# Performance work log

Measured on AMD Instinct MI355X. Metric: run time of the kernel, lower is better.

## Reference

```python
import jax, jax.numpy as jnp
import numpy as np

N = 50000
E = 800000
P = 400000
D_IN = 128
D_HID = 128


def setup_inputs() -> dict:
    key = jax.random.key(0)
    k = jax.random.split(key, 7)
    edge_index = jax.random.randint(k[0], (2, E), 0, N, dtype=jnp.int32)
    edge_pairs = jax.random.randint(k[1], (2, P), 0, N, dtype=jnp.int32)
    emb = jax.random.normal(k[2], (N, D_IN), dtype=jnp.float32)
    W1 = jax.random.normal(k[3], (D_IN, D_HID), dtype=jnp.float32) * (1.0 / np.sqrt(D_IN))
    b1 = jnp.zeros((D_HID,), dtype=jnp.float32)
    W2 = jax.random.normal(k[4], (D_HID, D_HID), dtype=jnp.float32) * (1.0 / np.sqrt(D_HID))
    b2 = jnp.zeros((D_HID,), dtype=jnp.float32)
    return {"edge_index": edge_index, "edge_pairs": edge_pairs, "emb": emb,
            "W1": W1, "b1": b1, "W2": W2, "b2": b2}


def gcn_conv(x, W, b, src, dst):
    """PyG GCNConv: add self-loops, symmetric deg^-1/2 normalization,
    linear transform, scatter-add aggregation into destination nodes."""
    n = x.shape[0]
    loop = jnp.arange(n, dtype=src.dtype)
    s = jnp.concatenate([src, loop])  # [E+N]
    d = jnp.concatenate([dst, loop])
    deg = jax.ops.segment_sum(jnp.ones_like(d, dtype=x.dtype), d, num_segments=n)
    dinv = jnp.where(deg > 0, jax.lax.rsqrt(jnp.maximum(deg, 1e-12)), 0.0)
    norm = dinv[s] * dinv[d]  # [E+N]
    h = x @ W  # [N, out]
    msg = h[s] * norm[:, None]  # gather + scale
    out = jax.ops.segment_sum(msg, d, num_segments=n)  # scatter-add
    return out + b


def reference(edge_index, edge_pairs, emb, W1, b1, W2, b2):
    src, dst = edge_index[0], edge_index[1]
    # encode (eval mode: dropout is identity)
    z = jax.nn.relu(gcn_conv(emb, W1, b1, src, dst))
    z = gcn_conv(z, W2, b2, src, dst)
    # decode: dot product per candidate pair
    return jnp.sum(z[edge_pairs[0]] * z[edge_pairs[1]], axis=1)  # [P]
```

## Files before the change

kernel.cpp:

```cpp
#include <hip/hip_runtime.h>


typedef __attribute__((ext_vector_type(8))) short short8;
typedef __attribute__((ext_vector_type(4))) float floatx4;

#define STAGE_G 128

__device__ __forceinline__ unsigned short f2bf(float f) {
    union { float f; unsigned int u; } v; v.f = f;
    unsigned int u = v.u;
    u += 0x7fffu + ((u >> 16) & 1u);
    return (unsigned short)(u >> 16);
}

__device__ __forceinline__ unsigned int pack2(float a, float b) {
    return (unsigned int)f2bf(a) | ((unsigned int)f2bf(b) << 16);
}

__device__ __forceinline__ float4 cvt4(unsigned int lo, unsigned int hi) {
    float4 f;
    f.x = __uint_as_float(lo << 16);
    f.y = __uint_as_float(lo & 0xffff0000u);
    f.z = __uint_as_float(hi << 16);
    f.w = __uint_as_float(hi & 0xffff0000u);
    return f;
}


__global__ __launch_bounds__(256) void block_hist_kernel(const int* __restrict__ dst,
                                                         int* __restrict__ bhist,
                                                         int E, int NB) {
    __shared__ int bh[1024];
    int t = threadIdx.x, g = blockIdx.x;
    for (int b = t; b < NB; b += 256) bh[b] = 0;
    __syncthreads();
    int chunk = (E + gridDim.x - 1) / gridDim.x;
    int lo = g * chunk, hi = min(lo + chunk, E);
    for (int i = lo + t; i < hi; i += 256) atomicAdd(&bh[dst[i] >> 6], 1);
    __syncthreads();
    for (int b = t; b < NB; b += 256) bhist[g * NB + b] = bh[b];
}

__global__ __launch_bounds__(128) void s1_scan_blocks(int* __restrict__ bhist,
                                                      int* __restrict__ T, int NB) {
    __shared__ int s[2][128];
    int b = blockIdx.x, t = threadIdx.x;
    int v = bhist[t * NB + b];
    int cur = 0;
    s[0][t] = v;
    __syncthreads();
#pragma unroll
    for (int off = 1; off < 128; off <<= 1) {
        int nxt = cur ^ 1;
        int val = s[cur][t];
        if (t >= off) val += s[cur][t - off];
        s[nxt][t] = val;
        __syncthreads();
        cur = nxt;
    }
    int inc = s[cur][t];
    bhist[t * NB + b] = inc - v;
    if (t == 127) T[b] = inc;
}

__global__ __launch_bounds__(256) void stage_kernel(const int* __restrict__ src,
                                                    const int* __restrict__ dst,
                                                    const int* __restrict__ bhist,
                                                    const int* __restrict__ T,
                                                    int* __restrict__ bucket_base,
                                                    unsigned int* __restrict__ stage,
                                                    int E, int NB) {
    __shared__ int lcur[1024];
    __shared__ int sb[2][256];
    int t = threadIdx.x, g = blockIdx.x;

    int b0 = t * 4;
    int v[4];
    int s = 0;
#pragma unroll
    for (int i = 0; i < 4; ++i) {
        int b = b0 + i;
        v[i] = (b < NB) ? T[b] : 0;
        s += v[i];
    }
    int cur = 0;
    sb[0][t] = s;
    __syncthreads();
#pragma unroll
    for (int off = 1; off < 256; off <<= 1) {
        int val = sb[cur][t];
        if (t >= off) val += sb[cur][t - off];
        sb[cur ^ 1][t] = val;
        __syncthreads();
        cur ^= 1;
    }
    int run = sb[cur][t] - s;
#pragma unroll
    for (int i = 0; i < 4; ++i) {
        int b = b0 + i;
        if (b < NB) {
            lcur[b] = run + bhist[(size_t)g * NB + b];
            if (g == 0) bucket_base[b] = run;
        }
        run += v[i];
    }
    if (g == 0 && t == 255) bucket_base[NB] = run;
    __syncthreads();

    int chunk = (E + gridDim.x - 1) / gridDim.x;
    int lo = g * chunk, hi = min(lo + chunk, E);
    for (int i = lo + t; i < hi; i += 256) {
        int d = dst[i];
        int pos = atomicAdd(&lcur[d >> 6], 1);
        stage[pos] = ((unsigned int)src[i] << 6) | (unsigned int)(d & 63);
    }
}

__global__ __launch_bounds__(256) void scatter_kernel(const unsigned int* __restrict__ stage,
                                                      const int* __restrict__ bucket_base,
                                                      int* __restrict__ row_ptr,
                                                      float* __restrict__ dinv,
                                                      int* __restrict__ srcs_sorted,
                                                      int N) {
    __shared__ int cnt[64];
    __shared__ int lcur[64];
    int b = blockIdx.x, t = threadIdx.x;
    int lo = b << 6;
    int base = bucket_base[b], basen = bucket_base[b + 1];
    if (t < 64) cnt[t] = 0;
    __syncthreads();
    for (int i = base + t; i < basen; i += 256) atomicAdd(&cnt[stage[i] & 63u], 1);
    __syncthreads();
    if (t < 64) {
        int v = cnt[t];
        int inc = v;
#pragma unroll
        for (int off = 1; off < 64; off <<= 1) {
            int x = __shfl_up(inc, off, 64);
            if (t >= off) inc += x;
        }
        int exc = inc - v;
        int node = lo + t;
        if (node < N) {
            row_ptr[node] = base + exc;
            dinv[node] = rsqrtf((float)(v + 1));
            if (node == N - 1) row_ptr[N] = base + exc + v;
        }
        lcur[t] = base + exc;
    }
    __syncthreads();
    for (int i = base + t; i < basen; i += 256) {
        unsigned int rec = stage[i];
        int pos = atomicAdd(&lcur[rec & 63u], 1);
        srcs_sorted[pos] = (int)(rec >> 6);
    }
}

__global__ __launch_bounds__(256) void gemm_mfma_kernel(const float* __restrict__ Xv,
                                                        const float* __restrict__ W,
                                                        const float* __restrict__ dinv,
                                                        uint2* __restrict__ H, int N) {
    __shared__ __align__(16) char smem[50176];
    short* WB = (short*)smem;
    short* XL = (short*)(smem + 32768);
    float* Cst = (float*)smem;

    const int tid = threadIdx.x;
    const int w = tid >> 6;
    const int lane = tid & 63;
    const int blk = blockIdx.x;

    {
        const float4* W4 = (const float4*)W;
#pragma unroll
        for (int i = 0; i < 16; ++i) {
            int f = tid + i * 256;
            int k = f >> 5;
            int c4 = f & 31;
            float4 wv = W4[f];
            int kt = k >> 5, q = (k >> 3) & 3, j = k & 7;
            float e[4] = {wv.x, wv.y, wv.z, wv.w};
#pragma unroll
            for (int m = 0; m < 4; ++m) {
                int c = c4 * 4 + m;
                int nt = c >> 4;
                int ln = q * 16 + (c & 15);
                WB[((nt * 4 + kt) * 64 + ln) * 8 + j] = (short)f2bf(e[m]);
            }
        }
    }
    {
#pragma unroll
        for (int i = 0; i < 8; ++i) {
            int f = tid + i * 256;
            int row = f >> 5;
            int c4 = f & 31;
            int gr = min(blk * 64 + row, N - 1);
            float4 xv = ((const float4*)Xv)[(size_t)gr * 32 + c4];
            uint2 u;
            u.x = pack2(xv.x, xv.y);
            u.y = pack2(xv.z, xv.w);
            *(uint2*)&XL[row * 136 + c4 * 4] = u;
        }
    }
    __syncthreads();

    const int arow = w * 16 + (lane & 15);
    const int koff = (lane >> 4) * 8;
    short8 a[4];
#pragma unroll
    for (int kt = 0; kt < 4; ++kt)
        a[kt] = *(const short8*)&XL[arow * 136 + kt * 32 + koff];

    floatx4 acc[8];
#pragma unroll
    for (int nt = 0; nt < 8; ++nt) acc[nt] = (floatx4){0.f, 0.f, 0.f, 0.f};

#pragma unroll
    for (int kt = 0; kt < 4; ++kt) {
#pragma unroll
        for (int nt = 0; nt < 8; ++nt) {
            short8 b = *(const short8*)&WB[((nt * 4 + kt) * 64 + lane) * 8];
            acc[nt] = __builtin_amdgcn_mfma_f32_16x16x32_bf16(a[kt], b, acc[nt], 0, 0, 0);
        }
    }
    __syncthreads();

    {
        int q = lane >> 4, cn = lane & 15;
#pragma unroll
        for (int nt = 0; nt < 8; ++nt)
#pragma unroll
            for (int r = 0; r < 4; ++r)
                Cst[(w * 16 + q * 4 + r) * 132 + nt * 16 + cn] = acc[nt][r];
    }
    __syncthreads();
    {
#pragma unroll
        for (int i = 0; i < 8; ++i) {
            int f = tid + i * 256;
            int row = f >> 5;
            int c4 = f & 31;
            int gr = blk * 64 + row;
            if (gr < N) {
                float4 v = *(float4*)&Cst[row * 132 + c4 * 4];
                float di = dinv[gr];
                uint2 o;
                o.x = pack2(v.x * di, v.y * di);
                o.y = pack2(v.z * di, v.w * di);
                H[(size_t)gr * 32 + c4] = o;
            }
        }
    }
}

__global__ __launch_bounds__(256) void agg_gemm_kernel(const unsigned short* __restrict__ Hp,
                                                       const int* __restrict__ row_ptr,
                                                       const int* __restrict__ srcs,
                                                       const float* __restrict__ dinv,
                                                       const float* __restrict__ bias1,
                                                       const float* __restrict__ W2,
                                                       uint2* __restrict__ Hout, int N) {
    __shared__ __align__(16) char smem[50176];
    short* WB = (short*)smem;
    short* XL = (short*)(smem + 32768);
    float* Cst = (float*)smem;

    const int tid = threadIdx.x;
    const int blk = blockIdx.x;

    {
        const float4* W4 = (const float4*)W2;
#pragma unroll
        for (int i = 0; i < 16; ++i) {
            int f = tid + i * 256;
            int k = f >> 5;
            int c4 = f & 31;
            float4 wv = W4[f];
            int kt = k >> 5, q = (k >> 3) & 3, j = k & 7;
            float e[4] = {wv.x, wv.y, wv.z, wv.w};
#pragma unroll
            for (int m = 0; m < 4; ++m) {
                int c = c4 * 4 + m;
                int nt = c >> 4;
                int ln = q * 16 + (c & 15);
                WB[((nt * 4 + kt) * 64 + ln) * 8 + j] = (short)f2bf(e[m]);
            }
        }
    }

    {
        int qw = tid >> 4;
        int hl = tid & 15;
        const uint4* H4 = (const uint4*)Hp;
        float4 bv0 = ((const float4*)bias1)[2 * hl];
        float4 bv1 = ((const float4*)bias1)[2 * hl + 1];
#pragma unroll
        for (int r = 0; r < 4; ++r) {
            int idx = qw + 16 * r;
            int n = blk * 64 + idx;
            uint4 o;
            if (n < N) {
                uint4 us = H4[(size_t)n * 16 + hl];
                float4 a0 = cvt4(us.x, us.y);
                float4 a1 = cvt4(us.z, us.w);
                float4 c0 = make_float4(0.f, 0.f, 0.f, 0.f);
                float4 c1 = make_float4(0.f, 0.f, 0.f, 0.f);
                int j = row_ptr[n], end = row_ptr[n + 1];
                for (; j + 3 < end; j += 4) {
                    uint4 u0 = H4[(size_t)srcs[j + 0] * 16 + hl];
                    uint4 u1 = H4[(size_t)srcs[j + 1] * 16 + hl];
                    uint4 u2 = H4[(size_t)srcs[j + 2] * 16 + hl];
                    uint4 u3 = H4[(size_t)srcs[j + 3] * 16 + hl];
                    float4 t;
                    t = cvt4(u0.x, u0.y); a0.x += t.x; a0.y += t.y; a0.z += t.z; a0.w += t.w;
                    t = cvt4(u0.z, u0.w); a1.x += t.x; a1.y += t.y; a1.z += t.z; a1.w += t.w;
                    t = cvt4(u1.x, u1.y); c0.x += t.x; c0.y += t.y; c0.z += t.z; c0.w += t.w;
                    t = cvt4(u1.z, u1.w); c1.x += t.x; c1.y += t.y; c1.z += t.z; c1.w += t.w;
                    t = cvt4(u2.x, u2.y); a0.x += t.x; a0.y += t.y; a0.z += t.z; a0.w += t.w;
                    t = cvt4(u2.z, u2.w); a1.x += t.x; a1.y += t.y; a1.z += t.z; a1.w += t.w;
                    t = cvt4(u3.x, u3.y); c0.x += t.x; c0.y += t.y; c0.z += t.z; c0.w += t.w;
                    t = cvt4(u3.z, u3.w); c1.x += t.x; c1.y += t.y; c1.z += t.z; c1.w += t.w;
                }
                for (; j < end; ++j) {
                    uint4 u = H4[(size_t)srcs[j] * 16 + hl];
                    float4 t;
                    t = cvt4(u.x, u.y); a0.x += t.x; a0.y += t.y; a0.z += t.z; a0.w += t.w;
                    t = cvt4(u.z, u.w); a1.x += t.x; a1.y += t.y; a1.z += t.z; a1.w += t.w;
                }
                a0.x += c0.x; a0.y += c0.y; a0.z += c0.z; a0.w += c0.w;
                a1.x += c1.x; a1.y += c1.y; a1.z += c1.z; a1.w += c1.w;
                float di = dinv[n];
                float o0 = fmaxf(di * a0.x + bv0.x, 0.f);
                float o1 = fmaxf(di * a0.y + bv0.y, 0.f);
                float o2 = fmaxf(di * a0.z + bv0.z, 0.f);
                float o3 = fmaxf(di * a0.w + bv0.w, 0.f);
                float o4 = fmaxf(di * a1.x + bv1.x, 0.f);
                float o5 = fmaxf(di * a1.y + bv1.y, 0.f);
                float o6 = fmaxf(di * a1.z + bv1.z, 0.f);
                float o7 = fmaxf(di * a1.w + bv1.w, 0.f);
                o.x = pack2(o0, o1);
                o.y = pack2(o2, o3);
                o.z = pack2(o4, o5);
                o.w = pack2(o6, o7);
            } else {
                o = make_uint4(0u, 0u, 0u, 0u);
            }
            *(uint4*)&XL[idx * 136 + hl * 8] = o;
        }
    }
    __syncthreads();

    const int w = tid >> 6;
    const int lane = tid & 63;
    const int arow = w * 16 + (lane & 15);
    const int koff = (lane >> 4) * 8;
    short8 a[4];
#pragma unroll
    for (int kt = 0; kt < 4; ++kt)
        a[kt] = *(const short8*)&XL[arow * 136 + kt * 32 + koff];

    floatx4 acc[8];
#pragma unroll
    for (int nt = 0; nt < 8; ++nt) acc[nt] = (floatx4){0.f, 0.f, 0.f, 0.f};

#pragma unroll
    for (int kt = 0; kt < 4; ++kt) {
#pragma unroll
        for (int nt = 0; nt < 8; ++nt) {
            short8 b = *(const short8*)&WB[((nt * 4 + kt) * 64 + lane) * 8];
            acc[nt] = __builtin_amdgcn_mfma_f32_16x16x32_bf16(a[kt], b, acc[nt], 0, 0, 0);
        }
    }
    __syncthreads();

    {
        int q = lane >> 4, cn = lane & 15;
#pragma unroll
        for (int nt = 0; nt < 8; ++nt)
#pragma unroll
            for (int r = 0; r < 4; ++r)
                Cst[(w * 16 + q * 4 + r) * 132 + nt * 16 + cn] = acc[nt][r];
    }
    __syncthreads();
    {
#pragma unroll
        for (int i = 0; i < 8; ++i) {
            int f = tid + i * 256;
            int row = f >> 5;
            int c4 = f & 31;
            int gr = blk * 64 + row;
            if (gr < N) {
                float4 v = *(float4*)&Cst[row * 132 + c4 * 4];
                float di = dinv[gr];
                uint2 o;
                o.x = pack2(v.x * di, v.y * di);
                o.y = pack2(v.z * di, v.w * di);
                Hout[(size_t)gr * 32 + c4] = o;
            }
        }
    }
}

__global__ __launch_bounds__(256) void agg_kernel(const unsigned short* __restrict__ Hp,
                                                  const int* __restrict__ row_ptr,
                                                  const int* __restrict__ srcs,
                                                  const float* __restrict__ dinv,
                                                  const float* __restrict__ bias,
                                                  unsigned short* __restrict__ Z,
                                                  int N, int do_relu) {
    int gw = (int)((blockIdx.x * blockDim.x + threadIdx.x) >> 6);
    int lane = threadIdx.x & 63;
    int q = lane >> 4;
    int hl = lane & 15;
    int n = gw * 4 + q;
    if (n >= N) return;

    const uint4* H4 = (const uint4*)Hp;
    uint4 us = H4[(size_t)n * 16 + hl];
    float4 a0 = cvt4(us.x, us.y);
    float4 a1 = cvt4(us.z, us.w);
    float4 b0 = make_float4(0.f, 0.f, 0.f, 0.f);
    float4 b1 = make_float4(0.f, 0.f, 0.f, 0.f);

    int j = row_ptr[n], end = row_ptr[n + 1];
    for (; j + 7 < end; j += 8) {
        uint4 u0 = H4[(size_t)srcs[j + 0] * 16 + hl];
        uint4 u1 = H4[(size_t)srcs[j + 1] * 16 + hl];
        uint4 u2 = H4[(size_t)srcs[j + 2] * 16 + hl];
        uint4 u3 = H4[(size_t)srcs[j + 3] * 16 + hl];
        uint4 u4 = H4[(size_t)srcs[j + 4] * 16 + hl];
        uint4 u5 = H4[(size_t)srcs[j + 5] * 16 + hl];
        uint4 u6 = H4[(size_t)srcs[j + 6] * 16 + hl];
        uint4 u7 = H4[(size_t)srcs[j + 7] * 16 + hl];
        float4 t;
        t = cvt4(u0.x, u0.y); a0.x += t.x; a0.y += t.y; a0.z += t.z; a0.w += t.w;
        t = cvt4(u0.z, u0.w); a1.x += t.x; a1.y += t.y; a1.z += t.z; a1.w += t.w;
        t = cvt4(u1.x, u1.y); b0.x += t.x; b0.y += t.y; b0.z += t.z; b0.w += t.w;
        t = cvt4(u1.z, u1.w); b1.x += t.x; b1.y += t.y; b1.z += t.z; b1.w += t.w;
        t = cvt4(u2.x, u2.y); a0.x += t.x; a0.y += t.y; a0.z += t.z; a0.w += t.w;
        t = cvt4(u2.z, u2.w); a1.x += t.x; a1.y += t.y; a1.z += t.z; a1.w += t.w;
        t = cvt4(u3.x, u3.y); b0.x += t.x; b0.y += t.y; b0.z += t.z; b0.w += t.w;
        t = cvt4(u3.z, u3.w); b1.x += t.x; b1.y += t.y; b1.z += t.z; b1.w += t.w;
        t = cvt4(u4.x, u4.y); a0.x += t.x; a0.y += t.y; a0.z += t.z; a0.w += t.w;
        t = cvt4(u4.z, u4.w); a1.x += t.x; a1.y += t.y; a1.z += t.z; a1.w += t.w;
        t = cvt4(u5.x, u5.y); b0.x += t.x; b0.y += t.y; b0.z += t.z; b0.w += t.w;
        t = cvt4(u5.z, u5.w); b1.x += t.x; b1.y += t.y; b1.z += t.z; b1.w += t.w;
        t = cvt4(u6.x, u6.y); a0.x += t.x; a0.y += t.y; a0.z += t.z; a0.w += t.w;
        t = cvt4(u6.z, u6.w); a1.x += t.x; a1.y += t.y; a1.z += t.z; a1.w += t.w;
        t = cvt4(u7.x, u7.y); b0.x += t.x; b0.y += t.y; b0.z += t.z; b0.w += t.w;
        t = cvt4(u7.z, u7.w); b1.x += t.x; b1.y += t.y; b1.z += t.z; b1.w += t.w;
    }
    for (; j + 3 < end; j += 4) {
        uint4 u0 = H4[(size_t)srcs[j + 0] * 16 + hl];
        uint4 u1 = H4[(size_t)srcs[j + 1] * 16 + hl];
        uint4 u2 = H4[(size_t)srcs[j + 2] * 16 + hl];
        uint4 u3 = H4[(size_t)srcs[j + 3] * 16 + hl];
        float4 t;
        t = cvt4(u0.x, u0.y); a0.x += t.x; a0.y += t.y; a0.z += t.z; a0.w += t.w;
        t = cvt4(u0.z, u0.w); a1.x += t.x; a1.y += t.y; a1.z += t.z; a1.w += t.w;
        t = cvt4(u1.x, u1.y); b0.x += t.x; b0.y += t.y; b0.z += t.z; b0.w += t.w;
        t = cvt4(u1.z, u1.w); b1.x += t.x; b1.y += t.y; b1.z += t.z; b1.w += t.w;
        t = cvt4(u2.x, u2.y); a0.x += t.x; a0.y += t.y; a0.z += t.z; a0.w += t.w;
        t = cvt4(u2.z, u2.w); a1.x += t.x; a1.y += t.y; a1.z += t.z; a1.w += t.w;
        t = cvt4(u3.x, u3.y); b0.x += t.x; b0.y += t.y; b0.z += t.z; b0.w += t.w;
        t = cvt4(u3.z, u3.w); b1.x += t.x; b1.y += t.y; b1.z += t.z; b1.w += t.w;
    }
    for (; j < end; ++j) {
        uint4 u = H4[(size_t)srcs[j] * 16 + hl];
        float4 t;
        t = cvt4(u.x, u.y); a0.x += t.x; a0.y += t.y; a0.z += t.z; a0.w += t.w;
        t = cvt4(u.z, u.w); a1.x += t.x; a1.y += t.y; a1.z += t.z; a1.w += t.w;
    }
    a0.x += b0.x; a0.y += b0.y; a0.z += b0.z; a0.w += b0.w;
    a1.x += b1.x; a1.y += b1.y; a1.z += b1.z; a1.w += b1.w;

    float di = dinv[n];
    float4 bv0 = ((const float4*)bias)[2 * hl];
    float4 bv1 = ((const float4*)bias)[2 * hl + 1];
    float o0 = di * a0.x + bv0.x, o1 = di * a0.y + bv0.y;
    float o2 = di * a0.z + bv0.z, o3 = di * a0.w + bv0.w;
    float o4 = di * a1.x + bv1.x, o5 = di * a1.y + bv1.y;
    float o6 = di * a1.z + bv1.z, o7 = di * a1.w + bv1.w;
    if (do_relu) {
        o0 = fmaxf(o0, 0.f); o1 = fmaxf(o1, 0.f); o2 = fmaxf(o2, 0.f); o3 = fmaxf(o3, 0.f);
        o4 = fmaxf(o4, 0.f); o5 = fmaxf(o5, 0.f); o6 = fmaxf(o6, 0.f); o7 = fmaxf(o7, 0.f);
    }
    uint4 o;
    o.x = pack2(o0, o1);
    o.y = pack2(o2, o3);
    o.z = pack2(o4, o5);
    o.w = pack2(o6, o7);
    ((uint4*)Z)[(size_t)n * 16 + hl] = o;
}

__global__ __launch_bounds__(256) void decode_kernel(const unsigned short* __restrict__ Z,
                                                     const int* __restrict__ pa,
                                                     const int* __restrict__ pb,
                                                     float* __restrict__ out, int P) {
    int wv = (int)((blockIdx.x * blockDim.x + threadIdx.x) >> 6);
    int lane = threadIdx.x & 63;
    int q = lane >> 4;
    int hl = lane & 15;
    int p0 = wv * 8 + q * 2;
    if (p0 >= P) return;
    const uint4* Z4 = (const uint4*)Z;

    bool two = (p0 + 1 < P);
    int A0 = pa[p0], B0 = pb[p0];
    int A1 = two ? pa[p0 + 1] : A0;
    int B1 = two ? pb[p0 + 1] : B0;
    uint4 ua0 = Z4[(size_t)A0 * 16 + hl];
    uint4 ub0 = Z4[(size_t)B0 * 16 + hl];
    uint4 ua1 = Z4[(size_t)A1 * 16 + hl];
    uint4 ub1 = Z4[(size_t)B1 * 16 + hl];

    float4 xa, xb, ya, yb;
    xa = cvt4(ua0.x, ua0.y); xb = cvt4(ub0.x, ub0.y);
    ya = cvt4(ua0.z, ua0.w); yb = cvt4(ub0.z, ub0.w);
    float v0 = xa.x * xb.x + xa.y * xb.y + xa.z * xb.z + xa.w * xb.w
             + ya.x * yb.x + ya.y * yb.y + ya.z * yb.z + ya.w * yb.w;
    xa = cvt4(ua1.x, ua1.y); xb = cvt4(ub1.x, ub1.y);
    ya = cvt4(ua1.z, ua1.w); yb = cvt4(ub1.z, ub1.w);
    float v1 = xa.x * xb.x + xa.y * xb.y + xa.z * xb.z + xa.w * xb.w
             + ya.x * yb.x + ya.y * yb.y + ya.z * yb.z + ya.w * yb.w;
#pragma unroll
    for (int off = 8; off > 0; off >>= 1) {
        v0 += __shfl_down(v0, off, 16);
        v1 += __shfl_down(v1, off, 16);
    }
    if (hl == 0) {
        out[p0] = v0;
        if (two) out[p0 + 1] = v1;
    }
}

extern "C" void kernel_launch(void* const* d_in, const int* in_sizes, int n_in,
                              void* d_out, int out_size, void* d_ws, size_t ws_size,
                              hipStream_t stream) {
    const int*   edge_index = (const int*)d_in[0];
    const int*   edge_pairs = (const int*)d_in[1];
    const float* emb        = (const float*)d_in[2];
    const float* W1         = (const float*)d_in[3];
    const float* b1         = (const float*)d_in[4];
    const float* W2         = (const float*)d_in[5];
    const float* b2         = (const float*)d_in[6];
    float* out = (float*)d_out;

    int E = in_sizes[0] / 2;
    int P = in_sizes[1] / 2;
    int N = in_sizes[2] / 128;
    int NB = (N + 63) / 64;

    const int* src = edge_index;
    const int* dst = edge_index + E;
    const int* pa  = edge_pairs;
    const int* pb  = edge_pairs + P;

    char* ws = (char*)d_ws;
    size_t off = 0;
    auto alloc = [&](size_t bytes) -> void* {
        void* p = ws + off;
        off = (off + bytes + 255) & ~(size_t)255;
        return p;
    };
    unsigned short* bufA = (unsigned short*)alloc((size_t)N * 128 * 2);
    unsigned short* bufB = (unsigned short*)alloc((size_t)N * 128 * 2);
    int*   srcs_sorted  = (int*)alloc((size_t)E * sizeof(int));
    unsigned int* stage = (unsigned int*)alloc((size_t)E * sizeof(unsigned int));
    int*   row_ptr      = (int*)alloc((size_t)(N + 1) * sizeof(int));
    float* dinv         = (float*)alloc((size_t)N * sizeof(float));
    int*   bhist        = (int*)alloc((size_t)STAGE_G * NB * sizeof(int));
    int*   T            = (int*)alloc((size_t)NB * sizeof(int));
    int*   bucket_base  = (int*)alloc((size_t)(NB + 1) * sizeof(int));

    block_hist_kernel<<<STAGE_G, 256, 0, stream>>>(dst, bhist, E, NB);
    s1_scan_blocks<<<NB, 128, 0, stream>>>(bhist, T, NB);
    stage_kernel<<<STAGE_G, 256, 0, stream>>>(src, dst, bhist, T, bucket_base, stage, E, NB);
    scatter_kernel<<<NB, 256, 0, stream>>>(stage, bucket_base, row_ptr, dinv, srcs_sorted, N);

    gemm_mfma_kernel<<<(N + 63) / 64, 256, 0, stream>>>(emb, W1, dinv, (uint2*)bufA, N);

    agg_gemm_kernel<<<(N + 63) / 64, 256, 0, stream>>>(bufA, row_ptr, srcs_sorted, dinv,
                                                       b1, W2, (uint2*)bufB, N);

    agg_kernel<<<(N + 15) / 16, 256, 0, stream>>>(bufB, row_ptr, srcs_sorted, dinv, b2,
                                                  (unsigned short*)bufA, N, 0);

    decode_kernel<<<(P + 31) / 32, 256, 0, stream>>>((unsigned short*)bufA, pa, pb, out, P);
}
```

Baseline: 260.3 us.

## Fuse CSR scatter into first GEMM and split layer-2 aggregation from GEMM

Merges the CSR scatter kernel (row_ptr, dinv, sorted sources) into the first MFMA GEMM, so each 64-node block builds its bucket and then transforms the same 64 rows, reading dinv from shared memory. This removes one launch and a round trip of dinv through global memory. It also replaces the fused aggregate-plus-GEMM layer-1 kernel with a separate agg_kernel (relu, bf16 output) followed by a GEMM that reads bf16 input. The fused kernel's per-thread gather and poor occupancy are traded for an extra launch and an extra bf16 N×128 write and read.

```diff
diff --git a/kernel.cpp b/kernel.cpp
--- a/kernel.cpp
+++ b/kernel.cpp
@@ -116,59 +116,62 @@
     }
 }
 
-__global__ __launch_bounds__(256) void scatter_kernel(const unsigned int* __restrict__ stage,
-                                                      const int* __restrict__ bucket_base,
-                                                      int* __restrict__ row_ptr,
-                                                      float* __restrict__ dinv,
-                                                      int* __restrict__ srcs_sorted,
-                                                      int N) {
+__global__ __launch_bounds__(256) void scatter_gemm_kernel(const unsigned int* __restrict__ stage,
+                                                           const int* __restrict__ bucket_base,
+                                                           int* __restrict__ row_ptr,
+                                                           float* __restrict__ dinv,
+                                                           int* __restrict__ srcs_sorted,
+                                                           const float* __restrict__ Xv,
+                                                           const float* __restrict__ W,
+                                                           uint2* __restrict__ H, int N) {
+    __shared__ __align__(16) char smem[50176];
     __shared__ int cnt[64];
     __shared__ int lcur[64];
-    int b = blockIdx.x, t = threadIdx.x;
-    int lo = b << 6;
-    int base = bucket_base[b], basen = bucket_base[b + 1];
-    if (t < 64) cnt[t] = 0;
-    __syncthreads();
-    for (int i = base + t; i < basen; i += 256) atomicAdd(&cnt[stage[i] & 63u], 1);
-    __syncthreads();
-    if (t < 64) {
-        int v = cnt[t];
-        int inc = v;
-#pragma unroll
-        for (int off = 1; off < 64; off <<= 1) {
-            int x = __shfl_up(inc, off, 64);
-            if (t >= off) inc += x;
-        }
-        int exc = inc - v;
-        int node = lo + t;
-        if (node < N) {
-            row_ptr[node] = base + exc;
-            dinv[node] = rsqrtf((float)(v + 1));
-            if (node == N - 1) row_ptr[N] = base + exc + v;
-        }
-        lcur[t] = base + exc;
-    }
-    __syncthreads();
-    for (int i = base + t; i < basen; i += 256) {
-        unsigned int rec = stage[i];
-        int pos = atomicAdd(&lcur[rec & 63u], 1);
-        srcs_sorted[pos] = (int)(rec >> 6);
-    }
-}
-
-__global__ __launch_bounds__(256) void gemm_mfma_kernel(const float* __restrict__ Xv,
-                                                        const float* __restrict__ W,
-                                                        const float* __restrict__ dinv,
-                                                        uint2* __restrict__ H, int N) {
-    __shared__ __align__(16) char smem[50176];
+    __shared__ float sdinv[64];
     short* WB = (short*)smem;
     short* XL = (short*)(smem + 32768);
     float* Cst = (float*)smem;
 
     const int tid = threadIdx.x;
-    const int w = tid >> 6;
-    const int lane = tid & 63;
     const int blk = blockIdx.x;
+
+    {
+        int t = tid;
+        int lo = blk << 6;
+        int base = bucket_base[blk], basen = bucket_base[blk + 1];
+        if (t < 64) cnt[t] = 0;
+        __syncthreads();
+        for (int i = base + t; i < basen; i += 256) atomicAdd(&cnt[stage[i] & 63u], 1);
+        __syncthreads();
+        if (t < 64) {
+            int v = cnt[t];
+            int inc = v;
+#pragma unroll
+            for (int off = 1; off < 64; off <<= 1) {
+                int x = __shfl_up(inc, off, 64);
+                if (t >= off) inc += x;
+            }
+            int exc = inc - v;
+            int node = lo + t;
+            float di = rsqrtf((float)(v + 1));
+            if (node < N) {
+                row_ptr[node] = base + exc;
+                dinv[node] = di;
+                if (node == N - 1) row_ptr[N] = base + exc + v;
+                sdinv[t] = di;
+            } else {
+                sdinv[t] = 0.f;
+            }
+            lcur[t] = base + exc;
+        }
+        __syncthreads();
+        for (int i = base + t; i < basen; i += 256) {
+            unsigned int rec = stage[i];
+            int pos = atomicAdd(&lcur[rec & 63u], 1);
+            srcs_sorted[pos] = (int)(rec >> 6);
+        }
+    }
+    __syncthreads();
 
     {
         const float4* W4 = (const float4*)W;
@@ -200,6 +203,103 @@
             uint2 u;
             u.x = pack2(xv.x, xv.y);
             u.y = pack2(xv.z, xv.w);
+            *(uint2*)&XL[row * 136 + c4 * 4] = u;
+        }
+    }
+    __syncthreads();
+
+    const int w = tid >> 6;
+    const int lane = tid & 63;
+    const int arow = w * 16 + (lane & 15);
+    const int koff = (lane >> 4) * 8;
+    short8 a[4];
+#pragma unroll
+    for (int kt = 0; kt < 4; ++kt)
+        a[kt] = *(const short8*)&XL[arow * 136 + kt * 32 + koff];
+
+    floatx4 acc[8];
+#pragma unroll
+    for (int nt = 0; nt < 8; ++nt) acc[nt] = (floatx4){0.f, 0.f, 0.f, 0.f};
+
+#pragma unroll
+    for (int kt = 0; kt < 4; ++kt) {
+#pragma unroll
+        for (int nt = 0; nt < 8; ++nt) {
+            short8 b = *(const short8*)&WB[((nt * 4 + kt) * 64 + lane) * 8];
+            acc[nt] = __builtin_amdgcn_mfma_f32_16x16x32_bf16(a[kt], b, acc[nt], 0, 0, 0);
+        }
+    }
+    __syncthreads();
+
+    {
+        int q = lane >> 4, cn = lane & 15;
+#pragma unroll
+        for (int nt = 0; nt < 8; ++nt)
+#pragma unroll
+            for (int r = 0; r < 4; ++r)
+                Cst[(w * 16 + q * 4 + r) * 132 + nt * 16 + cn] = acc[nt][r];
+    }
+    __syncthreads();
+    {
+#pragma unroll
+        for (int i = 0; i < 8; ++i) {
+            int f = tid + i * 256;
+            int row = f >> 5;
+            int c4 = f & 31;
+            int gr = blk * 64 + row;
+            if (gr < N) {
+                float4 v = *(float4*)&Cst[row * 132 + c4 * 4];
+                float di = sdinv[row];
+                uint2 o;
+                o.x = pack2(v.x * di, v.y * di);
+                o.y = pack2(v.z * di, v.w * di);
+                H[(size_t)gr * 32 + c4] = o;
+            }
+        }
+    }
+}
+
+__global__ __launch_bounds__(256) void gemm_mfma_kernel(const unsigned short* __restrict__ Xv,
+                                                        const float* __restrict__ W,
+                                                        const float* __restrict__ dinv,
+                                                        uint2* __restrict__ H, int N) {
+    __shared__ __align__(16) char smem[50176];
+    short* WB = (short*)smem;
+    short* XL = (short*)(smem + 32768);
+    float* Cst = (float*)smem;
+
+    const int tid = threadIdx.x;
+    const int w = tid >> 6;
+    const int lane = tid & 63;
+    const int blk = blockIdx.x;
+
+    {
+        const float4* W4 = (const float4*)W;
+#pragma unroll
+        for (int i = 0; i < 16; ++i) {
+            int f = tid + i * 256;
+            int k = f >> 5;
+            int c4 = f & 31;
+            float4 wv = W4[f];
+            int kt = k >> 5, q = (k >> 3) & 3, j = k & 7;
+            float e[4] = {wv.x, wv.y, wv.z, wv.w};
+#pragma unroll
+            for (int m = 0; m < 4; ++m) {
+                int c = c4 * 4 + m;
+                int nt = c >> 4;
+                int ln = q * 16 + (c & 15);
+                WB[((nt * 4 + kt) * 64 + ln) * 8 + j] = (short)f2bf(e[m]);
+            }
+        }
+    }
+    {
+#pragma unroll
+        for (int i = 0; i < 8; ++i) {
+            int f = tid + i * 256;
+            int row = f >> 5;
+            int c4 = f & 31;
+            int gr = min(blk * 64 + row, N - 1);
+            uint2 u = ((const uint2*)Xv)[(size_t)gr * 32 + c4];
             *(uint2*)&XL[row * 136 + c4 * 4] = u;
         }
     }
@@ -249,154 +349,6 @@
                 o.x = pack2(v.x * di, v.y * di);
                 o.y = pack2(v.z * di, v.w * di);
                 H[(size_t)gr * 32 + c4] = o;
-            }
-        }
-    }
-}
-
-__global__ __launch_bounds__(256) void agg_gemm_kernel(const unsigned short* __restrict__ Hp,
-                                                       const int* __restrict__ row_ptr,
-                                                       const int* __restrict__ srcs,
-                                                       const float* __restrict__ dinv,
-                                                       const float* __restrict__ bias1,
-                                                       const float* __restrict__ W2,
-                                                       uint2* __restrict__ Hout, int N) {
-    __shared__ __align__(16) char smem[50176];
-    short* WB = (short*)smem;
-    short* XL = (short*)(smem + 32768);
-    float* Cst = (float*)smem;
-
-    const int tid = threadIdx.x;
-    const int blk = blockIdx.x;
-
-    {
-        const float4* W4 = (const float4*)W2;
-#pragma unroll
-        for (int i = 0; i < 16; ++i) {
-            int f = tid + i * 256;
-            int k = f >> 5;
-            int c4 = f & 31;
-            float4 wv = W4[f];
-            int kt = k >> 5, q = (k >> 3) & 3, j = k & 7;
-            float e[4] = {wv.x, wv.y, wv.z, wv.w};
-#pragma unroll
-            for (int m = 0; m < 4; ++m) {
-                int c = c4 * 4 + m;
-                int nt = c >> 4;
-                int ln = q * 16 + (c & 15);
-                WB[((nt * 4 + kt) * 64 + ln) * 8 + j] = (short)f2bf(e[m]);
-            }
-        }
-    }
-
-    {
-        int qw = tid >> 4;
-        int hl = tid & 15;
-        const uint4* H4 = (const uint4*)Hp;
-        float4 bv0 = ((const float4*)bias1)[2 * hl];
-        float4 bv1 = ((const float4*)bias1)[2 * hl + 1];
-#pragma unroll
-        for (int r = 0; r < 4; ++r) {
-            int idx = qw + 16 * r;
-            int n = blk * 64 + idx;
-            uint4 o;
-            if (n < N) {
-                uint4 us = H4[(size_t)n * 16 + hl];
-                float4 a0 = cvt4(us.x, us.y);
-                float4 a1 = cvt4(us.z, us.w);
-                float4 c0 = make_float4(0.f, 0.f, 0.f, 0.f);
-                float4 c1 = make_float4(0.f, 0.f, 0.f, 0.f);
-                int j = row_ptr[n], end = row_ptr[n + 1];
-                for (; j + 3 < end; j += 4) {
-                    uint4 u0 = H4[(size_t)srcs[j + 0] * 16 + hl];
-                    uint4 u1 = H4[(size_t)srcs[j + 1] * 16 + hl];
-                    uint4 u2 = H4[(size_t)srcs[j + 2] * 16 + hl];
-                    uint4 u3 = H4[(size_t)srcs[j + 3] * 16 + hl];
-                    float4 t;
-                    t = cvt4(u0.x, u0.y); a0.x += t.x; a0.y += t.y; a0.z += t.z; a0.w += t.w;
-                    t = cvt4(u0.z, u0.w); a1.x += t.x; a1.y += t.y; a1.z += t.z; a1.w += t.w;
-                    t = cvt4(u1.x, u1.y); c0.x += t.x; c0.y += t.y; c0.z += t.z; c0.w += t.w;
-                    t = cvt4(u1.z, u1.w); c1.x += t.x; c1.y += t.y; c1.z += t.z; c1.w += t.w;
-                    t = cvt4(u2.x, u2.y); a0.x += t.x; a0.y += t.y; a0.z += t.z; a0.w += t.w;
-                    t = cvt4(u2.z, u2.w); a1.x += t.x; a1.y += t.y; a1.z += t.z; a1.w += t.w;
-                    t = cvt4(u3.x, u3.y); c0.x += t.x; c0.y += t.y; c0.z += t.z; c0.w += t.w;
-                    t = cvt4(u3.z, u3.w); c1.x += t.x; c1.y += t.y; c1.z += t.z; c1.w += t.w;
-                }
-                for (; j < end; ++j) {
-                    uint4 u = H4[(size_t)srcs[j] * 16 + hl];
-                    float4 t;
-                    t = cvt4(u.x, u.y); a0.x += t.x; a0.y += t.y; a0.z += t.z; a0.w += t.w;
-                    t = cvt4(u.z, u.w); a1.x += t.x; a1.y += t.y; a1.z += t.z; a1.w += t.w;
-                }
-                a0.x += c0.x; a0.y += c0.y; a0.z += c0.z; a0.w += c0.w;
-                a1.x += c1.x; a1.y += c1.y; a1.z += c1.z; a1.w += c1.w;
-                float di = dinv[n];
-                float o0 = fmaxf(di * a0.x + bv0.x, 0.f);
-                float o1 = fmaxf(di * a0.y + bv0.y, 0.f);
-                float o2 = fmaxf(di * a0.z + bv0.z, 0.f);
-                float o3 = fmaxf(di * a0.w + bv0.w, 0.f);
-                float o4 = fmaxf(di * a1.x + bv1.x, 0.f);
-                float o5 = fmaxf(di * a1.y + bv1.y, 0.f);
-                float o6 = fmaxf(di * a1.z + bv1.z, 0.f);
-                float o7 = fmaxf(di * a1.w + bv1.w, 0.f);
-                o.x = pack2(o0, o1);
-                o.y = pack2(o2, o3);
-                o.z = pack2(o4, o5);
-                o.w = pack2(o6, o7);
-            } else {
-                o = make_uint4(0u, 0u, 0u, 0u);
-            }
-            *(uint4*)&XL[idx * 136 + hl * 8] = o;
-        }
-    }
-    __syncthreads();
-
-    const int w = tid >> 6;
-    const int lane = tid & 63;
-    const int arow = w * 16 + (lane & 15);
-    const int koff = (lane >> 4) * 8;
-    short8 a[4];
-#pragma unroll
-    for (int kt = 0; kt < 4; ++kt)
-        a[kt] = *(const short8*)&XL[arow * 136 + kt * 32 + koff];
-
-    floatx4 acc[8];
-#pragma unroll
-    for (int nt = 0; nt < 8; ++nt) acc[nt] = (floatx4){0.f, 0.f, 0.f, 0.f};
-
-#pragma unroll
-    for (int kt = 0; kt < 4; ++kt) {
-#pragma unroll
-        for (int nt = 0; nt < 8; ++nt) {
-            short8 b = *(const short8*)&WB[((nt * 4 + kt) * 64 + lane) * 8];
-            acc[nt] = __builtin_amdgcn_mfma_f32_16x16x32_bf16(a[kt], b, acc[nt], 0, 0, 0);
-        }
-    }
-    __syncthreads();
-
-    {
-        int q = lane >> 4, cn = lane & 15;
-#pragma unroll
-        for (int nt = 0; nt < 8; ++nt)
-#pragma unroll
-            for (int r = 0; r < 4; ++r)
-                Cst[(w * 16 + q * 4 + r) * 132 + nt * 16 + cn] = acc[nt][r];
-    }
-    __syncthreads();
-    {
-#pragma unroll
-        for (int i = 0; i < 8; ++i) {
-            int f = tid + i * 256;
-            int row = f >> 5;
-            int c4 = f & 31;
-            int gr = blk * 64 + row;
-            if (gr < N) {
-                float4 v = *(float4*)&Cst[row * 132 + c4 * 4];
-                float di = dinv[gr];
-                uint2 o;
-                o.x = pack2(v.x * di, v.y * di);
-                o.y = pack2(v.z * di, v.w * di);
-                Hout[(size_t)gr * 32 + c4] = o;
             }
         }
     }
@@ -577,15 +529,17 @@
     block_hist_kernel<<<STAGE_G, 256, 0, stream>>>(dst, bhist, E, NB);
     s1_scan_blocks<<<NB, 128, 0, stream>>>(bhist, T, NB);
     stage_kernel<<<STAGE_G, 256, 0, stream>>>(src, dst, bhist, T, bucket_base, stage, E, NB);
-    scatter_kernel<<<NB, 256, 0, stream>>>(stage, bucket_base, row_ptr, dinv, srcs_sorted, N);
-
-    gemm_mfma_kernel<<<(N + 63) / 64, 256, 0, stream>>>(emb, W1, dinv, (uint2*)bufA, N);
-
-    agg_gemm_kernel<<<(N + 63) / 64, 256, 0, stream>>>(bufA, row_ptr, srcs_sorted, dinv,
-                                                       b1, W2, (uint2*)bufB, N);
-
-    agg_kernel<<<(N + 15) / 16, 256, 0, stream>>>(bufB, row_ptr, srcs_sorted, dinv, b2,
-                                                  (unsigned short*)bufA, N, 0);
-
-    decode_kernel<<<(P + 31) / 32, 256, 0, stream>>>((unsigned short*)bufA, pa, pb, out, P);
-}
+
+    scatter_gemm_kernel<<<NB, 256, 0, stream>>>(stage, bucket_base, row_ptr, dinv,
+                                                srcs_sorted, emb, W1, (uint2*)bufA, N);
+
+    agg_kernel<<<(N + 15) / 16, 256, 0, stream>>>(bufA, row_ptr, srcs_sorted, dinv, b1,
+                                                  bufB, N, 1);
+
+    gemm_mfma_kernel<<<NB, 256, 0, stream>>>(bufB, W2, dinv, (uint2*)bufA, N);
+
+    agg_kernel<<<(N + 15) / 16, 256, 0, stream>>>(bufA, row_ptr, srcs_sorted, dinv, b2,
+                                                  bufB, N, 0);
+
+    decode_kernel<<<(P + 31) / 32, 256, 0, stream>>>(bufB, pa, pb, out, P);
+}
```

After: 248.0 us. -4.7%, faster.
